# Kernel tuning notes

Measured on AMD Instinct MI355X. Metric: run time of the kernel, lower is better.

The kernel has to match this reference:

```python
import jax, jax.numpy as jnp
import numpy as np
from jax import lax
from jax.scipy.special import logsumexp

B, T, N = 256, 512, 128


def setup_inputs() -> dict:
    key = jax.random.key(0)
    k1, k2, k3 = jax.random.split(key, 3)
    emissions = jax.random.normal(k1, (B, T, N), dtype=jnp.float32)
    tag_ids = jax.random.randint(k2, (B, T), 0, N, dtype=jnp.int64)
    mask = jnp.ones((B, T), dtype=jnp.int32)
    # learned transition matrix (glorot-uniform-ish init)
    limit = float(np.sqrt(6.0 / (N + N)))
    trans = jax.random.uniform(k3, (N, N), minval=-limit, maxval=limit, dtype=jnp.float32)
    return {"emissions": emissions, "tag_ids": tag_ids, "mask": mask, "trans": trans}


def _sequence_score(emissions, tag_ids, maskf, trans):
    # unary: emission score of the gold tag at each valid step
    unary = jnp.take_along_axis(emissions, tag_ids[:, :, None], axis=2)[..., 0]  # [B,T]
    unary = jnp.sum(unary * maskf, axis=1)
    # binary: transition score between consecutive gold tags
    binary = trans[tag_ids[:, :-1], tag_ids[:, 1:]] * maskf[:, 1:]  # [B,T-1]
    return unary + jnp.sum(binary, axis=1)


def _log_norm(emissions, maskf, trans):
    # forward algorithm over time via lax.scan; alpha: [B,N]
    alpha0 = emissions[:, 0]
    em = jnp.swapaxes(emissions, 0, 1)[1:]   # [T-1,B,N]
    mk = jnp.swapaxes(maskf, 0, 1)[1:]       # [T-1,B]

    def step(alpha, xs):
        emit_t, m_t = xs
        new = logsumexp(alpha[:, :, None] + trans[None], axis=1) + emit_t
        alpha = jnp.where(m_t[:, None] > 0, new, alpha)
        return alpha, None

    alpha, _ = lax.scan(step, alpha0, (em, mk))
    return logsumexp(alpha, axis=1)  # [B]


def _viterbi_decode(emissions, maskf, trans):
    alpha0 = emissions[:, 0]
    em = jnp.swapaxes(emissions, 0, 1)[1:]
    mk = jnp.swapaxes(maskf, 0, 1)[1:]
    idx = jnp.arange(N, dtype=jnp.int32)[None]

    def fwd(alpha, xs):
        emit_t, m_t = xs
        scores = alpha[:, :, None] + trans[None]        # [B,N,N]
        bp = jnp.argmax(scores, axis=1).astype(jnp.int32)  # [B,N]
        new = jnp.max(scores, axis=1) + emit_t
        valid = m_t[:, None] > 0
        alpha = jnp.where(valid, new, alpha)
        bp = jnp.where(valid, bp, idx)  # carry same tag through padding
        return alpha, bp

    alpha, bps = lax.scan(fwd, alpha0, (em, mk))  # bps: [T-1,B,N]
    last_tag = jnp.argmax(alpha, axis=1).astype(jnp.int32)  # [B]

    def bwd(tag, bp_t):
        new_tag = jnp.take_along_axis(bp_t, tag[:, None], axis=1)[:, 0]
        return new_tag, new_tag

    _, tags_rev = lax.scan(bwd, last_tag, bps[::-1])  # [T-1,B]
    tags = jnp.concatenate([tags_rev[::-1], last_tag[None]], axis=0)  # [T,B]
    return jnp.swapaxes(tags, 0, 1)  # [B,T]


def reference(emissions, tag_ids, mask, trans):
    maskf = mask.astype(emissions.dtype)
    log_likelihood = _sequence_score(emissions, tag_ids, maskf, trans) - _log_norm(emissions, maskf, trans)
    predict = _viterbi_decode(emissions, maskf, trans)
    return (log_likelihood, trans, predict)
```

## Files before the change

### kernel.cpp

```cpp
#include <hip/hip_runtime.h>
#include <cmath>

#define BB 256
#define TT 512
#define NN 128
#define LN2F 0.6931471805599453f

typedef __bf16 bf16x8 __attribute__((ext_vector_type(8)));
typedef float floatx4 __attribute__((ext_vector_type(4)));

__device__ __forceinline__ float wave_max64(float v) {
    #pragma unroll
    for (int off = 32; off; off >>= 1) v = fmaxf(v, __shfl_xor(v, off));
    return v;
}
__device__ __forceinline__ float wave_sum64(float v) {
    #pragma unroll
    for (int off = 32; off; off >>= 1) v += __shfl_xor(v, off);
    return v;
}
__device__ __forceinline__ int wave_argmax128(float v0, float v1, int l) {
    float m = fmaxf(v0, v1);
    float wm = wave_max64(m);
    unsigned long long ball = __ballot(m == wm);
    int lane = __ffsll(ball) - 1;
    int idx = (v0 == wm) ? (2 * l) : (2 * l + 1);
    return __shfl(idx, lane);
}

__device__ __forceinline__ __bf16 to_bf16(float f) {
    unsigned u = __float_as_uint(f);
    unsigned r = (u + 0x7FFFu + ((u >> 16) & 1u)) >> 16;
    union { unsigned short s; __bf16 b; } cv;
    cv.s = (unsigned short)r;
    return cv.b;
}

__device__ __forceinline__ float dpp_xor1_f(float v) {
    return __int_as_float(__builtin_amdgcn_mov_dpp(__float_as_int(v), 0xB1, 0xF, 0xF, true));
}
__device__ __forceinline__ int dpp_xor1_i(int v) {
    return __builtin_amdgcn_mov_dpp(v, 0xB1, 0xF, 0xF, true);
}

__device__ __forceinline__ int padidx64(int i) { return 68 * (i >> 6) + (i & 63); }

__global__ __launch_bounds__(256, 2) void fwd_kernel(
        const float* __restrict__ em, const int* __restrict__ gtags,
        const int* __restrict__ mask, const float* __restrict__ trans,
        float* __restrict__ out_ll, float* __restrict__ out_trans,
        float* __restrict__ outp) {
    const int bi = blockIdx.x;
    const bool isV = bi < BB;
    const int b = isV ? bi : bi - BB;
    const int tid = threadIdx.x;
    const int w = tid >> 6;
    const int l = tid & 63;

    __shared__ __align__(16) float stA[136], stB[136];
    __shared__ __align__(16) __bf16 sbf[2][NN];
    __shared__ unsigned char bp_lds[TT * NN];
    __shared__ unsigned char tags_lds[TT];
    __shared__ unsigned char map_lds[4 * NN];
    __shared__ int entry_sh[4];
    __shared__ int msk[TT];
    __shared__ float piv[2];
    __shared__ float sfin[NN];
    __shared__ float wsum[4];
    __shared__ float llnorm_sh;
    __shared__ int misc[2];

    msk[tid] = mask[b * TT + tid];
    msk[tid + 256] = mask[b * TT + tid + 256];

    const float* emb = em + (size_t)b * TT * NN;

    if (isV) {
        __builtin_amdgcn_s_setprio(1);
        const int jv = tid >> 1;
        const int qv = tid & 1;
        const int i0 = 64 * qv;
        float4 C[16];
        {
            const float* tc = trans + (size_t)i0 * NN + jv;
            #pragma unroll
            for (int u = 0; u < 16; ++u) {
                C[u].x = tc[(size_t)(4*u+0) * NN];
                C[u].y = tc[(size_t)(4*u+1) * NN];
                C[u].z = tc[(size_t)(4*u+2) * NN];
                C[u].w = tc[(size_t)(4*u+3) * NN];
            }
        }
        float st;
        {
            float a0 = emb[jv];
            st = a0;
            if (qv == 0) stA[padidx64(jv)] = a0;
        }
        float e_next = emb[NN + jv];
        __syncthreads();

        unsigned long long mb = __ballot(msk[l] != 0);

        const float4* apA = (const float4*)(stA + 68 * qv);
        const float4* apB = (const float4*)(stB + 68 * qv);

        auto VSTEP = [&](int t, const float4* ap, float* dst) {
            if ((t & 63) == 0) mb = __ballot(msk[t + l] != 0);
            const int m = (int)((mb >> (t & 63)) & 1ULL);
            const float e_cur = e_next;
            if (t + 1 < TT) e_next = emb[(size_t)(t + 1) * NN + jv];
            float4 vv[16];
            #pragma unroll
            for (int u = 0; u < 16; ++u) vv[u] = ap[u];
            float m0 = -INFINITY, m1 = -INFINITY, m2 = -INFINITY, m3 = -INFINITY;
            int u0 = 0, u1 = 0, u2 = 0, u3 = 0;
            #pragma unroll
            for (int u = 0; u < 16; ++u) {
                float a = vv[u].x + C[u].x; u0 = (a > m0) ? u : u0; m0 = fmaxf(m0, a);
                float bq = vv[u].y + C[u].y; u1 = (bq > m1) ? u : u1; m1 = fmaxf(m1, bq);
                float c = vv[u].z + C[u].z; u2 = (c > m2) ? u : u2; m2 = fmaxf(m2, c);
                float d = vv[u].w + C[u].w; u3 = (d > m3) ? u : u3; m3 = fmaxf(m3, d);
            }
            float bv = m0; int bx = i0 + 4 * u0;
            { int id = i0 + 4*u1 + 1; if (m1 > bv || (m1 == bv && id < bx)) { bv = m1; bx = id; } }
            { int id = i0 + 4*u2 + 2; if (m2 > bv || (m2 == bv && id < bx)) { bv = m2; bx = id; } }
            { int id = i0 + 4*u3 + 3; if (m3 > bv || (m3 == bv && id < bx)) { bv = m3; bx = id; } }
            {
                float ov = dpp_xor1_f(bv); int oi = dpp_xor1_i(bx);
                if (ov > bv || (ov == bv && oi < bx)) { bv = ov; bx = oi; }
            }
            if (qv == 0) {
                float an; int bp;
                if (m) { an = bv + e_cur; bp = bx; }
                else   { an = st;         bp = jv; }
                st = an;
                dst[padidx64(jv)] = an;
                bp_lds[t * NN + jv] = (unsigned char)bp;
            }
            __syncthreads();
        };

        for (int t = 1; t < TT - 1; t += 2) {
            VSTEP(t, apA, stB);
            VSTEP(t + 1, apB, stA);
        }
        VSTEP(TT - 1, apA, stB);

        if (w == 0) {
            float a0 = stB[padidx64(2 * l)], a1 = stB[padidx64(2 * l + 1)];
            int tg = wave_argmax128(a0, a1, l);
            if (l == 0) { misc[0] = tg; tags_lds[TT - 1] = (unsigned char)tg; }
        }
        if (tid < 64) out_trans[b * 64 + tid] = trans[b * 64 + tid];
        __syncthreads();
        const int lo = 128 * w + 1;
        const int hi = (w == 3) ? (TT - 1) : (128 * w + 128);
        {
            int tA = 2 * l, tB = 2 * l + 1;
            for (int t = hi; t >= lo; --t) {
                tA = bp_lds[t * NN + tA];
                tB = bp_lds[t * NN + tB];
            }
            map_lds[w * NN + 2 * l]     = (unsigned char)tA;
            map_lds[w * NN + 2 * l + 1] = (unsigned char)tB;
        }
        __syncthreads();
        if (tid == 0) {
            int e = misc[0];
            entry_sh[3] = e;
            for (int c = 3; c >= 1; --c) { e = map_lds[c * NN + e]; entry_sh[c - 1] = e; }
        }
        __syncthreads();
        if (l == 0) {
            int tg = entry_sh[w];
            for (int t = hi; t >= lo; --t) {
                tg = bp_lds[t * NN + tg];
                tags_lds[t - 1] = (unsigned char)tg;
            }
        }
        __syncthreads();
        outp[(size_t)b * TT + tid]       = (float)tags_lds[tid];
        outp[(size_t)b * TT + tid + 256] = (float)tags_lds[tid + 256];
        __builtin_amdgcn_s_setprio(0);
    } else {
        const int q = l >> 4;
        const int j0 = (l & 15) + 32 * w;
        const int j1 = j0 + 16;
        bf16x8 Bf0[4], Bf1[4];
        #pragma unroll
        for (int kc = 0; kc < 4; ++kc) {
            #pragma unroll
            for (int jj = 0; jj < 8; ++jj) {
                int row = kc * 32 + q * 8 + jj;
                Bf0[kc][jj] = to_bf16(__expf(trans[(size_t)row * NN + j0]));
                Bf1[kc][jj] = to_bf16(__expf(trans[(size_t)row * NN + j1]));
            }
        }
        float ss0 = __expf(emb[j0]);
        float ss1 = __expf(emb[j1]);
        int kacc = 0;
        if (l < 16) { sbf[0][j0] = to_bf16(ss0); sbf[0][j1] = to_bf16(ss1); }
        if (tid == 0) piv[0] = ss0;
        float e0_next = emb[NN + j0];
        float e1_next = emb[NN + j1];
        __syncthreads();

        for (int t = 1; t < TT; ++t) {
            const float e0_cur = e0_next, e1_cur = e1_next;
            if (t + 1 < TT) {
                e0_next = emb[(size_t)(t + 1) * NN + j0];
                e1_next = emb[(size_t)(t + 1) * NN + j1];
            }
            const int m = msk[t];
            const int p = (t - 1) & 1, qb = t & 1;
            if (m) {
                const __bf16* sp = sbf[p];
                floatx4 acc0 = {0.f, 0.f, 0.f, 0.f};
                floatx4 acc1 = {0.f, 0.f, 0.f, 0.f};
                #pragma unroll
                for (int kc = 0; kc < 4; ++kc) {
                    bf16x8 a = *(const bf16x8*)(sp + kc * 32 + q * 8);
                    acc0 = __builtin_amdgcn_mfma_f32_16x16x32_bf16(a, Bf0[kc], acc0, 0, 0, 0);
                    acc1 = __builtin_amdgcn_mfma_f32_16x16x32_bf16(a, Bf1[kc], acc1, 0, 0, 0);
                }
                const float pv = piv[p];
                const int k = (int)(__float_as_uint(pv) >> 23) - 127;
                const float scale = __uint_as_float((unsigned)(127 - k) << 23);
                ss0 = acc0[0] * scale * __expf(e0_cur);
                ss1 = acc1[0] * scale * __expf(e1_cur);
                if (tid == 0) kacc += k;
            }
            if (l < 16) { sbf[qb][j0] = to_bf16(ss0); sbf[qb][j1] = to_bf16(ss1); }
            if (tid == 0) piv[qb] = ss0;
            __syncthreads();
        }

        if (l < 16) { sfin[j0] = ss0; sfin[j1] = ss1; }
        if (tid == 0) misc[1] = kacc;
        __syncthreads();
        if (w == 0) {
            float v = sfin[2 * l] + sfin[2 * l + 1];
            v = wave_sum64(v);
            if (l == 0) llnorm_sh = __logf(v) + (float)misc[1] * LN2F;
        }
        float acc = 0.f;
        #pragma unroll
        for (int rep = 0; rep < 2; ++rep) {
            int t = tid + rep * 256;
            int tg = gtags[b * TT + t];
            float mf = (float)msk[t];
            acc += em[((size_t)b * TT + t) * NN + tg] * mf;
            if (t >= 1) {
                int tp = gtags[b * TT + t - 1];
                acc += trans[tp * NN + tg] * mf;
            }
        }
        acc = wave_sum64(acc);
        if (l == 0) wsum[w] = acc;
        __syncthreads();
        if (tid == 0) {
            float s = 0.f;
            #pragma unroll
            for (int i = 0; i < 4; ++i) s += wsum[i];
            out_ll[b] = s - llnorm_sh;
        }
    }
}

extern "C" void kernel_launch(void* const* d_in, const int* in_sizes, int n_in,
                              void* d_out, int out_size, void* d_ws, size_t ws_size,
                              hipStream_t stream) {
    const float* em = (const float*)d_in[0];
    const int* gtags = (const int*)d_in[1];
    const int* mask = (const int*)d_in[2];
    const float* trans = (const float*)d_in[3];

    float* out = (float*)d_out;
    float* out_ll = out;
    float* out_trans = out + BB;
    float* out_pred = out + BB + NN * NN;

    hipLaunchKernelGGL(fwd_kernel, dim3(2 * BB), dim3(256), 0, stream,
                       em, gtags, mask, trans, out_ll, out_trans, out_pred);
}
```

Before: 580.2 us.

## Merge Viterbi and forward-algorithm blocks into one 512-thread block per sequence

Instead of launching separate blocks for the Viterbi max-product recursion and the log-partition forward recursion, each block now has 512 threads. Waves 0-3 run Viterbi and waves 4-7 run the MFMA-based forward pass, sharing one __syncthreads per timestep. This halves the block count and shares the mask and LDS setup, and the two halves can overlap inside a CU. In exchange, each step now waits on both recursions through the shared barrier, and occupancy and register limits change under launch_bounds(512,4).

```diff
diff --git a/kernel.cpp b/kernel.cpp
--- a/kernel.cpp
+++ b/kernel.cpp
@@ -45,17 +45,16 @@
 
 __device__ __forceinline__ int padidx64(int i) { return 68 * (i >> 6) + (i & 63); }
 
-__global__ __launch_bounds__(256, 2) void fwd_kernel(
+__global__ __launch_bounds__(512, 4) void fwd_kernel(
         const float* __restrict__ em, const int* __restrict__ gtags,
         const int* __restrict__ mask, const float* __restrict__ trans,
         float* __restrict__ out_ll, float* __restrict__ out_trans,
         float* __restrict__ outp) {
-    const int bi = blockIdx.x;
-    const bool isV = bi < BB;
-    const int b = isV ? bi : bi - BB;
+    const int b = blockIdx.x;
     const int tid = threadIdx.x;
     const int w = tid >> 6;
     const int l = tid & 63;
+    const bool isV = (w < 4);
 
     __shared__ __align__(16) float stA[136], stB[136];
     __shared__ __align__(16) __bf16 sbf[2][NN];
@@ -71,45 +70,64 @@
     __shared__ int misc[2];
 
     msk[tid] = mask[b * TT + tid];
-    msk[tid + 256] = mask[b * TT + tid + 256];
-
     const float* emb = em + (size_t)b * TT * NN;
+
+    const int jv = tid >> 1;
+    const int qv = tid & 1;
+    const int i0 = 64 * qv;
+    float4 C[16];
+    float st = 0.f, e_next = 0.f;
+    const int sw = w - 4;
+    const int q = l >> 4;
+    bf16x8 Bf[2][4];
+    float ss[2], es_next[2];
+    int kacc = 0;
 
     if (isV) {
         __builtin_amdgcn_s_setprio(1);
-        const int jv = tid >> 1;
-        const int qv = tid & 1;
-        const int i0 = 64 * qv;
-        float4 C[16];
-        {
-            const float* tc = trans + (size_t)i0 * NN + jv;
+        const float* tc = trans + (size_t)i0 * NN + jv;
+        #pragma unroll
+        for (int u = 0; u < 16; ++u) {
+            C[u].x = tc[(size_t)(4*u+0) * NN];
+            C[u].y = tc[(size_t)(4*u+1) * NN];
+            C[u].z = tc[(size_t)(4*u+2) * NN];
+            C[u].w = tc[(size_t)(4*u+3) * NN];
+        }
+        float a0 = emb[jv];
+        st = a0;
+        if (qv == 0) stA[padidx64(jv)] = a0;
+        e_next = emb[NN + jv];
+    } else {
+        #pragma unroll
+        for (int g = 0; g < 2; ++g) {
+            const int j = (l & 15) + 16 * (2 * sw + g);
             #pragma unroll
-            for (int u = 0; u < 16; ++u) {
-                C[u].x = tc[(size_t)(4*u+0) * NN];
-                C[u].y = tc[(size_t)(4*u+1) * NN];
-                C[u].z = tc[(size_t)(4*u+2) * NN];
-                C[u].w = tc[(size_t)(4*u+3) * NN];
-            }
-        }
-        float st;
-        {
-            float a0 = emb[jv];
-            st = a0;
-            if (qv == 0) stA[padidx64(jv)] = a0;
-        }
-        float e_next = emb[NN + jv];
-        __syncthreads();
-
-        unsigned long long mb = __ballot(msk[l] != 0);
-
-        const float4* apA = (const float4*)(stA + 68 * qv);
-        const float4* apB = (const float4*)(stB + 68 * qv);
-
-        auto VSTEP = [&](int t, const float4* ap, float* dst) {
+            for (int kc = 0; kc < 4; ++kc) {
+                #pragma unroll
+                for (int jj = 0; jj < 8; ++jj) {
+                    int row = kc * 32 + q * 8 + jj;
+                    Bf[g][kc][jj] = to_bf16(__expf(trans[(size_t)row * NN + j]));
+                }
+            }
+            ss[g] = __expf(emb[j]);
+            if (l < 16) sbf[0][j] = to_bf16(ss[g]);
+            es_next[g] = emb[NN + j];
+        }
+        if (tid == 256) piv[0] = ss[0];
+    }
+    __syncthreads();
+
+    unsigned long long mb = isV ? __ballot(msk[l] != 0) : 0ULL;
+
+    for (int t = 1; t < TT; ++t) {
+        if (isV) {
             if ((t & 63) == 0) mb = __ballot(msk[t + l] != 0);
             const int m = (int)((mb >> (t & 63)) & 1ULL);
             const float e_cur = e_next;
             if (t + 1 < TT) e_next = emb[(size_t)(t + 1) * NN + jv];
+            const float* src = (t & 1) ? stA : stB;
+            float* dst = (t & 1) ? stB : stA;
+            const float4* ap = (const float4*)(src + 68 * qv);
             float4 vv[16];
             #pragma unroll
             for (int u = 0; u < 16; ++u) vv[u] = ap[u];
@@ -138,134 +156,116 @@
                 dst[padidx64(jv)] = an;
                 bp_lds[t * NN + jv] = (unsigned char)bp;
             }
-            __syncthreads();
-        };
-
-        for (int t = 1; t < TT - 1; t += 2) {
-            VSTEP(t, apA, stB);
-            VSTEP(t + 1, apB, stA);
-        }
-        VSTEP(TT - 1, apA, stB);
-
-        if (w == 0) {
-            float a0 = stB[padidx64(2 * l)], a1 = stB[padidx64(2 * l + 1)];
-            int tg = wave_argmax128(a0, a1, l);
-            if (l == 0) { misc[0] = tg; tags_lds[TT - 1] = (unsigned char)tg; }
-        }
-        if (tid < 64) out_trans[b * 64 + tid] = trans[b * 64 + tid];
-        __syncthreads();
-        const int lo = 128 * w + 1;
-        const int hi = (w == 3) ? (TT - 1) : (128 * w + 128);
-        {
-            int tA = 2 * l, tB = 2 * l + 1;
-            for (int t = hi; t >= lo; --t) {
-                tA = bp_lds[t * NN + tA];
-                tB = bp_lds[t * NN + tB];
-            }
-            map_lds[w * NN + 2 * l]     = (unsigned char)tA;
-            map_lds[w * NN + 2 * l + 1] = (unsigned char)tB;
-        }
-        __syncthreads();
-        if (tid == 0) {
-            int e = misc[0];
-            entry_sh[3] = e;
-            for (int c = 3; c >= 1; --c) { e = map_lds[c * NN + e]; entry_sh[c - 1] = e; }
-        }
-        __syncthreads();
-        if (l == 0) {
-            int tg = entry_sh[w];
-            for (int t = hi; t >= lo; --t) {
-                tg = bp_lds[t * NN + tg];
-                tags_lds[t - 1] = (unsigned char)tg;
-            }
-        }
-        __syncthreads();
-        outp[(size_t)b * TT + tid]       = (float)tags_lds[tid];
-        outp[(size_t)b * TT + tid + 256] = (float)tags_lds[tid + 256];
-        __builtin_amdgcn_s_setprio(0);
-    } else {
-        const int q = l >> 4;
-        const int j0 = (l & 15) + 32 * w;
-        const int j1 = j0 + 16;
-        bf16x8 Bf0[4], Bf1[4];
-        #pragma unroll
-        for (int kc = 0; kc < 4; ++kc) {
-            #pragma unroll
-            for (int jj = 0; jj < 8; ++jj) {
-                int row = kc * 32 + q * 8 + jj;
-                Bf0[kc][jj] = to_bf16(__expf(trans[(size_t)row * NN + j0]));
-                Bf1[kc][jj] = to_bf16(__expf(trans[(size_t)row * NN + j1]));
-            }
-        }
-        float ss0 = __expf(emb[j0]);
-        float ss1 = __expf(emb[j1]);
-        int kacc = 0;
-        if (l < 16) { sbf[0][j0] = to_bf16(ss0); sbf[0][j1] = to_bf16(ss1); }
-        if (tid == 0) piv[0] = ss0;
-        float e0_next = emb[NN + j0];
-        float e1_next = emb[NN + j1];
-        __syncthreads();
-
-        for (int t = 1; t < TT; ++t) {
-            const float e0_cur = e0_next, e1_cur = e1_next;
-            if (t + 1 < TT) {
-                e0_next = emb[(size_t)(t + 1) * NN + j0];
-                e1_next = emb[(size_t)(t + 1) * NN + j1];
-            }
+        } else {
             const int m = msk[t];
             const int p = (t - 1) & 1, qb = t & 1;
+            float e_cur0 = es_next[0], e_cur1 = es_next[1];
+            if (t + 1 < TT) {
+                es_next[0] = emb[(size_t)(t + 1) * NN + (l & 15) + 16 * (2 * sw)];
+                es_next[1] = emb[(size_t)(t + 1) * NN + (l & 15) + 16 * (2 * sw + 1)];
+            }
             if (m) {
                 const __bf16* sp = sbf[p];
-                floatx4 acc0 = {0.f, 0.f, 0.f, 0.f};
-                floatx4 acc1 = {0.f, 0.f, 0.f, 0.f};
-                #pragma unroll
-                for (int kc = 0; kc < 4; ++kc) {
-                    bf16x8 a = *(const bf16x8*)(sp + kc * 32 + q * 8);
-                    acc0 = __builtin_amdgcn_mfma_f32_16x16x32_bf16(a, Bf0[kc], acc0, 0, 0, 0);
-                    acc1 = __builtin_amdgcn_mfma_f32_16x16x32_bf16(a, Bf1[kc], acc1, 0, 0, 0);
-                }
+                bf16x8 a0 = *(const bf16x8*)(sp + 0 * 32 + q * 8);
+                bf16x8 a1 = *(const bf16x8*)(sp + 1 * 32 + q * 8);
+                bf16x8 a2 = *(const bf16x8*)(sp + 2 * 32 + q * 8);
+                bf16x8 a3 = *(const bf16x8*)(sp + 3 * 32 + q * 8);
                 const float pv = piv[p];
                 const int k = (int)(__float_as_uint(pv) >> 23) - 127;
                 const float scale = __uint_as_float((unsigned)(127 - k) << 23);
-                ss0 = acc0[0] * scale * __expf(e0_cur);
-                ss1 = acc1[0] * scale * __expf(e1_cur);
-                if (tid == 0) kacc += k;
-            }
-            if (l < 16) { sbf[qb][j0] = to_bf16(ss0); sbf[qb][j1] = to_bf16(ss1); }
-            if (tid == 0) piv[qb] = ss0;
-            __syncthreads();
-        }
-
-        if (l < 16) { sfin[j0] = ss0; sfin[j1] = ss1; }
-        if (tid == 0) misc[1] = kacc;
+                {
+                    floatx4 acc = {0.f, 0.f, 0.f, 0.f};
+                    acc = __builtin_amdgcn_mfma_f32_16x16x32_bf16(a0, Bf[0][0], acc, 0, 0, 0);
+                    acc = __builtin_amdgcn_mfma_f32_16x16x32_bf16(a1, Bf[0][1], acc, 0, 0, 0);
+                    acc = __builtin_amdgcn_mfma_f32_16x16x32_bf16(a2, Bf[0][2], acc, 0, 0, 0);
+                    acc = __builtin_amdgcn_mfma_f32_16x16x32_bf16(a3, Bf[0][3], acc, 0, 0, 0);
+                    ss[0] = acc[0] * scale * __expf(e_cur0);
+                }
+                {
+                    floatx4 acc = {0.f, 0.f, 0.f, 0.f};
+                    acc = __builtin_amdgcn_mfma_f32_16x16x32_bf16(a0, Bf[1][0], acc, 0, 0, 0);
+                    acc = __builtin_amdgcn_mfma_f32_16x16x32_bf16(a1, Bf[1][1], acc, 0, 0, 0);
+                    acc = __builtin_amdgcn_mfma_f32_16x16x32_bf16(a2, Bf[1][2], acc, 0, 0, 0);
+                    acc = __builtin_amdgcn_mfma_f32_16x16x32_bf16(a3, Bf[1][3], acc, 0, 0, 0);
+                    ss[1] = acc[0] * scale * __expf(e_cur1);
+                }
+                if (tid == 256) kacc += k;
+            }
+            if (l < 16) {
+                sbf[qb][(l & 15) + 16 * (2 * sw)]     = to_bf16(ss[0]);
+                sbf[qb][(l & 15) + 16 * (2 * sw + 1)] = to_bf16(ss[1]);
+            }
+            if (tid == 256) piv[qb] = ss[0];
+        }
         __syncthreads();
-        if (w == 0) {
+    }
+
+    if (w == 0) {
+        float a0 = stB[padidx64(2 * l)], a1 = stB[padidx64(2 * l + 1)];
+        int tg = wave_argmax128(a0, a1, l);
+        if (l == 0) { misc[0] = tg; tags_lds[TT - 1] = (unsigned char)tg; }
+    }
+    if (!isV && l < 16) {
+        sfin[(l & 15) + 16 * (2 * sw)]     = ss[0];
+        sfin[(l & 15) + 16 * (2 * sw + 1)] = ss[1];
+    }
+    if (tid == 256) misc[1] = kacc;
+    if (tid < 64) out_trans[b * 64 + tid] = trans[b * 64 + tid];
+    __syncthreads();
+
+    float score_acc = 0.f;
+    if (isV) {
+        const int lo = 128 * w + 1;
+        const int hi = (w == 3) ? (TT - 1) : (128 * w + 128);
+        int tA = 2 * l, tB = 2 * l + 1;
+        for (int t = hi; t >= lo; --t) {
+            tA = bp_lds[t * NN + tA];
+            tB = bp_lds[t * NN + tB];
+        }
+        map_lds[w * NN + 2 * l]     = (unsigned char)tA;
+        map_lds[w * NN + 2 * l + 1] = (unsigned char)tB;
+    } else {
+        if (w == 4) {
             float v = sfin[2 * l] + sfin[2 * l + 1];
             v = wave_sum64(v);
             if (l == 0) llnorm_sh = __logf(v) + (float)misc[1] * LN2F;
         }
-        float acc = 0.f;
         #pragma unroll
         for (int rep = 0; rep < 2; ++rep) {
-            int t = tid + rep * 256;
+            int t = (tid - 256) + rep * 256;
             int tg = gtags[b * TT + t];
             float mf = (float)msk[t];
-            acc += em[((size_t)b * TT + t) * NN + tg] * mf;
+            score_acc += em[((size_t)b * TT + t) * NN + tg] * mf;
             if (t >= 1) {
                 int tp = gtags[b * TT + t - 1];
-                acc += trans[tp * NN + tg] * mf;
-            }
-        }
-        acc = wave_sum64(acc);
-        if (l == 0) wsum[w] = acc;
-        __syncthreads();
-        if (tid == 0) {
-            float s = 0.f;
-            #pragma unroll
-            for (int i = 0; i < 4; ++i) s += wsum[i];
-            out_ll[b] = s - llnorm_sh;
-        }
-    }
+                score_acc += trans[tp * NN + tg] * mf;
+            }
+        }
+        score_acc = wave_sum64(score_acc);
+        if (l == 0) wsum[sw] = score_acc;
+    }
+    __syncthreads();
+    if (tid == 0) {
+        int e = misc[0];
+        entry_sh[3] = e;
+        for (int c = 3; c >= 1; --c) { e = map_lds[c * NN + e]; entry_sh[c - 1] = e; }
+    }
+    if (tid == 256) {
+        float s = wsum[0] + wsum[1] + wsum[2] + wsum[3];
+        out_ll[b] = s - llnorm_sh;
+    }
+    __syncthreads();
+    if (isV && l == 0) {
+        const int lo = 128 * w + 1;
+        const int hi = (w == 3) ? (TT - 1) : (128 * w + 128);
+        int tg = entry_sh[w];
+        for (int t = hi; t >= lo; --t) {
+            tg = bp_lds[t * NN + tg];
+            tags_lds[t - 1] = (unsigned char)tg;
+        }
+    }
+    __syncthreads();
+    outp[(size_t)b * TT + tid] = (float)tags_lds[tid];
 }
 
 extern "C" void kernel_launch(void* const* d_in, const int* in_sizes, int n_in,
@@ -281,6 +281,6 @@
     float* out_trans = out + BB;
     float* out_pred = out + BB + NN * NN;
 
-    hipLaunchKernelGGL(fwd_kernel, dim3(2 * BB), dim3(256), 0, stream,
+    hipLaunchKernelGGL(fwd_kernel, dim3(BB), dim3(512), 0, stream,
                        em, gtags, mask, trans, out_ll, out_trans, out_pred);
 }
```

After: 1.488 ms. 2.56x slower.
